# Kernel tuning notes

Measured on AMD Instinct MI355X. Metric: run time of the kernel, lower is better.

The kernel has to match this reference:

```python
import jax, jax.numpy as jnp
import numpy as np

B, CIN, COUT, T, K = 8, 64, 64, 16384, 127


def setup_inputs() -> dict:
    key = jax.random.key(0)
    kx, kw = jax.random.split(key)
    x = jax.random.normal(kx, (B, CIN, T), dtype=jnp.float32)
    sigma = np.sqrt(2.0 / (CIN * K + COUT)).astype(np.float32)
    W = jax.random.normal(kw, (COUT, CIN, K), dtype=jnp.float32) * sigma
    return {"x": x, "W": W}


def reference(x, W):
    # Full linear convolution via FFT (true convolution, matches
    # torchaudio.functional.fftconvolve), summed over in_channels,
    # then trimmed to mode='same' (output length == T, centered).
    T_ = x.shape[-1]
    K_ = W.shape[-1]
    n = T_ + K_ - 1  # linear-conv length, no circular wraparound
    Xf = jnp.fft.rfft(x, n=n)   # [B, Cin, nf] complex
    Wf = jnp.fft.rfft(W, n=n)   # [Cout, Cin, nf] complex
    # Batched complex multiply-accumulate over in_channels (single pass,
    # no per-output-channel redundant FFTs).
    Yf = jnp.einsum('bif,oif->bof', Xf, Wf)  # [B, Cout, nf]
    y_full = jnp.fft.irfft(Yf, n=n)          # [B, Cout, T+K-1]
    start = (K_ - 1) // 2                    # 'same': centered crop
    return y_full[..., start:start + T_]
```

## Files before the change

kernel.cpp:

```cpp
#include <hip/hip_runtime.h>

#define T_LEN 16384
#define CIN   64
#define COUT  64
#define KTAPS 127
#define TN    256
#define WROWS 383
#define WT_KS 4096

typedef __attribute__((ext_vector_type(8)))  __bf16 bf16x8;
typedef __attribute__((ext_vector_type(16))) float  f32x16;
typedef __attribute__((ext_vector_type(4)))  float  float4v;

__device__ inline unsigned short f2bf(float f) {
    unsigned u = __builtin_bit_cast(unsigned, f);
    u += 0x7fffu + ((u >> 16) & 1u);
    return (unsigned short)(u >> 16);
}

__global__ void wt_transform(const float* __restrict__ W,
                             unsigned short* __restrict__ Wt) {
    int tid = blockIdx.x * 256 + threadIdx.x;
    int o = tid >> 6, i = tid & 63;
    int j = i ^ ((o & 7) << 3);
    const float* src = W + tid * KTAPS;
    unsigned short* dst = Wt + o * 64 + j;
    for (int kp = 0; kp < KTAPS; ++kp)
        dst[kp * WT_KS] = f2bf(src[126 - kp]);
}

#define GLL16(g, l)                                                        \
    __builtin_amdgcn_global_load_lds(                                      \
        (const __attribute__((address_space(1))) void*)(g),                \
        (__attribute__((address_space(3))) void*)(l), 16, 0, 0)

__global__ __launch_bounds__(256, 2)
void conv_mfma(const float* __restrict__ x,
               const unsigned short* __restrict__ Wt,
               float* __restrict__ y) {
    __shared__ unsigned short xs[WROWS * 64];
    __shared__ unsigned short as_[2][WT_KS];

    const int tid = threadIdx.x;
    const int bb  = blockIdx.x >> 6;
    const int tt  = blockIdx.x & 63;
    const int t0  = tt * TN;

    {
        const int cin  = tid >> 2;
        const int wseg = (tid & 3) * 96;
        const float* xrow = x + (bb * CIN + cin) * T_LEN + (t0 - 64);
        for (int j = 0; j < 96; j += 4) {
            const int w = wseg + j;
            const int u = t0 - 64 + w;
            float4v v;
            if (u >= 0 && u + 3 < T_LEN) {
                v = *(const float4v*)(xrow + w);
            } else {
                v.x = (u + 0 >= 0 && u + 0 < T_LEN) ? xrow[w + 0] : 0.f;
                v.y = (u + 1 >= 0 && u + 1 < T_LEN) ? xrow[w + 1] : 0.f;
                v.z = (u + 2 >= 0 && u + 2 < T_LEN) ? xrow[w + 2] : 0.f;
                v.w = (u + 3 >= 0 && u + 3 < T_LEN) ? xrow[w + 3] : 0.f;
            }
            #pragma unroll
            for (int e = 0; e < 4; ++e) {
                const int we = w + e;
                if (we < WROWS) {
                    const float fv = (e == 0) ? v.x : (e == 1) ? v.y : (e == 2) ? v.z : v.w;
                    xs[we * 64 + (cin ^ ((we & 7) << 3))] = f2bf(fv);
                }
            }
        }
    }
    __syncthreads();

    const int lane   = tid & 63;
    const int wv     = tid >> 6;
    const int l31    = lane & 31;
    const int kg     = lane >> 5;
    const int twbase = wv * 64;
    const int h2     = kg ^ (l31 & 7);
    const int brow0  = twbase + l31 + 1;

    auto stageA = [&](int kp, unsigned short* buf) {
        const char* g = (const char*)(Wt + kp * WT_KS) + wv * 2048 + lane * 16;
        char* l = (char*)buf + wv * 2048 + lane * 16;
        GLL16(g, l);
        GLL16(g + 1024, l + 1024);
    };

    stageA(0, as_[0]);
    asm volatile("s_waitcnt vmcnt(0)" ::: "memory");
    __builtin_amdgcn_s_barrier();

    f32x16 acc[2][2] = {};

    for (int kp = 0; kp < KTAPS; ++kp) {
        const unsigned short* abuf = as_[kp & 1];
        if (kp + 1 < KTAPS) stageA(kp + 1, as_[(kp & 1) ^ 1]);

        const int w0    = brow0 + kp;
        const int h     = kg ^ (w0 & 7);
        const int base0 = w0 * 64;
        #pragma unroll
        for (int cc = 0; cc < 4; ++cc) {
            const int ach = (((cc << 1) ^ h2) << 3);
            bf16x8 a0 = *(const bf16x8*)(abuf + l31 * 64 + ach);
            bf16x8 a1 = *(const bf16x8*)(abuf + (l31 + 32) * 64 + ach);
            const int coff = (((cc << 1) ^ h) << 3);
            bf16x8 b0 = *(const bf16x8*)(xs + base0 + coff);
            bf16x8 b1 = *(const bf16x8*)(xs + base0 + 2048 + coff);
            acc[0][0] = __builtin_amdgcn_mfma_f32_32x32x16_bf16(a0, b0, acc[0][0], 0, 0, 0);
            acc[0][1] = __builtin_amdgcn_mfma_f32_32x32x16_bf16(a0, b1, acc[0][1], 0, 0, 0);
            acc[1][0] = __builtin_amdgcn_mfma_f32_32x32x16_bf16(a1, b0, acc[1][0], 0, 0, 0);
            acc[1][1] = __builtin_amdgcn_mfma_f32_32x32x16_bf16(a1, b1, acc[1][1], 0, 0, 0);
        }

        asm volatile("s_waitcnt vmcnt(0) lgkmcnt(0)" ::: "memory");
        __builtin_amdgcn_s_barrier();
    }

    const int ybase = (bb * COUT) * T_LEN;
    #pragma unroll
    for (int m = 0; m < 2; ++m) {
        #pragma unroll
        for (int n = 0; n < 2; ++n) {
            const int t = t0 + twbase + n * 32 + l31;
            #pragma unroll
            for (int r = 0; r < 16; ++r) {
                const int o = m * 32 + (r & 3) + 8 * (r >> 2) + 4 * kg;
                y[ybase + o * T_LEN + t] = acc[m][n][r];
            }
        }
    }
}

extern "C" void kernel_launch(void* const* d_in, const int* in_sizes, int n_in,
                              void* d_out, int out_size, void* d_ws, size_t ws_size,
                              hipStream_t stream) {
    const float* x = (const float*)d_in[0];
    const float* W = (const float*)d_in[1];
    float* yout = (float*)d_out;
    unsigned short* Wt = (unsigned short*)d_ws;

    wt_transform<<<16, 256, 0, stream>>>(W, Wt);

    const int grid = 8 * (T_LEN / TN);
    conv_mfma<<<grid, 256, 0, stream>>>(x, Wt, yout);
}
```

Baseline: 139.7 us.

## Double time tile per block and widen per-wave output tile to 64x128

Each block now covers 512 time steps instead of 256, and each wave computes a 2x4 grid of 32x32 MFMA tiles instead of 2x2. This reuses each A (weight) fragment across four B fragments and halves the number of weight tiles staged per output. The LDS swizzle changes to 4-element groups XORed with a 16-row pattern, fragments are assembled from two 8-byte loads, and the tap loop is unrolled by two with constant buffer indices. The trade-off is more accumulator registers, which forces occupancy down to one block per CU, and only 256 blocks in the grid.

```diff
diff --git a/kernel.cpp b/kernel.cpp
--- a/kernel.cpp
+++ b/kernel.cpp
@@ -4,8 +4,8 @@
 #define CIN   64
 #define COUT  64
 #define KTAPS 127
-#define TN    256
-#define WROWS 383
+#define TN    512
+#define XROWS 640
 #define WT_KS 4096
 
 typedef __attribute__((ext_vector_type(8)))  __bf16 bf16x8;
@@ -22,9 +22,9 @@
                              unsigned short* __restrict__ Wt) {
     int tid = blockIdx.x * 256 + threadIdx.x;
     int o = tid >> 6, i = tid & 63;
-    int j = i ^ ((o & 7) << 3);
+    int hw = o * 64 + (((i >> 2) ^ (o & 15)) << 2) + (i & 3);
     const float* src = W + tid * KTAPS;
-    unsigned short* dst = Wt + o * 64 + j;
+    unsigned short* dst = Wt + hw;
     for (int kp = 0; kp < KTAPS; ++kp)
         dst[kp * WT_KS] = f2bf(src[126 - kp]);
 }
@@ -34,97 +34,120 @@
         (const __attribute__((address_space(1))) void*)(g),                \
         (__attribute__((address_space(3))) void*)(l), 16, 0, 0)
 
-__global__ __launch_bounds__(256, 2)
+__global__ __launch_bounds__(256, 1)
 void conv_mfma(const float* __restrict__ x,
                const unsigned short* __restrict__ Wt,
                float* __restrict__ y) {
-    __shared__ unsigned short xs[WROWS * 64];
     __shared__ unsigned short as_[2][WT_KS];
+    __shared__ unsigned short xs[XROWS * 64];
 
     const int tid = threadIdx.x;
-    const int bb  = blockIdx.x >> 6;
-    const int tt  = blockIdx.x & 63;
+    const int bb  = blockIdx.x >> 5;
+    const int tt  = blockIdx.x & 31;
     const int t0  = tt * TN;
 
     {
-        const int cin  = tid >> 2;
-        const int wseg = (tid & 3) * 96;
-        const float* xrow = x + (bb * CIN + cin) * T_LEN + (t0 - 64);
-        for (int j = 0; j < 96; j += 4) {
-            const int w = wseg + j;
+        const int cin = tid >> 2;
+        const int s   = tid & 3;
+        const float* xrow = x + (bb * CIN + cin) * T_LEN;
+        const int p = cin >> 2, c3 = cin & 3;
+        for (int j = 0; j < 40; ++j) {
+            const int w = 16 * j + 4 * s;
             const int u = t0 - 64 + w;
             float4v v;
-            if (u >= 0 && u + 3 < T_LEN) {
-                v = *(const float4v*)(xrow + w);
+            if (u >= 0 && u + 4 <= T_LEN) {
+                v = *(const float4v*)(xrow + u);
             } else {
-                v.x = (u + 0 >= 0 && u + 0 < T_LEN) ? xrow[w + 0] : 0.f;
-                v.y = (u + 1 >= 0 && u + 1 < T_LEN) ? xrow[w + 1] : 0.f;
-                v.z = (u + 2 >= 0 && u + 2 < T_LEN) ? xrow[w + 2] : 0.f;
-                v.w = (u + 3 >= 0 && u + 3 < T_LEN) ? xrow[w + 3] : 0.f;
+                v.x = (u + 0 >= 0 && u + 0 < T_LEN) ? xrow[u + 0] : 0.f;
+                v.y = (u + 1 >= 0 && u + 1 < T_LEN) ? xrow[u + 1] : 0.f;
+                v.z = (u + 2 >= 0 && u + 2 < T_LEN) ? xrow[u + 2] : 0.f;
+                v.w = (u + 3 >= 0 && u + 3 < T_LEN) ? xrow[u + 3] : 0.f;
             }
             #pragma unroll
             for (int e = 0; e < 4; ++e) {
                 const int we = w + e;
-                if (we < WROWS) {
-                    const float fv = (e == 0) ? v.x : (e == 1) ? v.y : (e == 2) ? v.z : v.w;
-                    xs[we * 64 + (cin ^ ((we & 7) << 3))] = f2bf(fv);
-                }
+                const float fv = (e == 0) ? v.x : (e == 1) ? v.y : (e == 2) ? v.z : v.w;
+                xs[we * 64 + ((p ^ (we & 15)) << 2) + c3] = f2bf(fv);
             }
         }
     }
+
+    auto stageA = [&](int kp, int buf) {
+        const char* g = (const char*)(Wt + kp * WT_KS) + tid * 16;
+        char* l = (char*)(&as_[buf][0]) + tid * 16;
+        GLL16(g, l);
+        GLL16(g + 4096, l + 4096);
+    };
+
+    stageA(0, 0);
+    asm volatile("s_waitcnt vmcnt(0)" ::: "memory");
     __syncthreads();
 
     const int lane   = tid & 63;
     const int wv     = tid >> 6;
     const int l31    = lane & 31;
     const int kg     = lane >> 5;
-    const int twbase = wv * 64;
-    const int h2     = kg ^ (l31 & 7);
+    const int twbase = wv * 128;
     const int brow0  = twbase + l31 + 1;
 
-    auto stageA = [&](int kp, unsigned short* buf) {
-        const char* g = (const char*)(Wt + kp * WT_KS) + wv * 2048 + lane * 16;
-        char* l = (char*)buf + wv * 2048 + lane * 16;
-        GLL16(g, l);
-        GLL16(g + 1024, l + 1024);
+    int aoff[2][4][2];
+    #pragma unroll
+    for (int m = 0; m < 2; ++m)
+        #pragma unroll
+        for (int cc = 0; cc < 4; ++cc)
+            #pragma unroll
+            for (int h = 0; h < 2; ++h)
+                aoff[m][cc][h] = (l31 + 32 * m) * 128 +
+                                 (((4 * cc + 2 * kg + h) ^ (l31 & 15)) << 3);
+
+    const char* asbase = (const char*)&as_[0][0];
+    const char* xsbase = (const char*)&xs[0];
+
+    f32x16 acc[2][4] = {};
+
+    auto tap = [&](int kp, int buf) {
+        if (kp + 1 < KTAPS) stageA(kp + 1, buf ^ 1);
+        const int rb   = brow0 + kp;
+        const int rb15 = rb & 15;
+        const char* arow = asbase + buf * 8192;
+        const char* xrowp = xsbase + rb * 128;
+        #pragma unroll
+        for (int cc = 0; cc < 4; ++cc) {
+            bf16x8 a[2];
+            #pragma unroll
+            for (int m = 0; m < 2; ++m) {
+                uint2 lo = *(const uint2*)(arow + aoff[m][cc][0]);
+                uint2 hi = *(const uint2*)(arow + aoff[m][cc][1]);
+                uint4 t4 = {lo.x, lo.y, hi.x, hi.y};
+                a[m] = __builtin_bit_cast(bf16x8, t4);
+            }
+            const int o0 = (((4 * cc + 2 * kg + 0) ^ rb15) << 3);
+            const int o1 = (((4 * cc + 2 * kg + 1) ^ rb15) << 3);
+            #pragma unroll
+            for (int n = 0; n < 4; ++n) {
+                uint2 lo = *(const uint2*)(xrowp + n * 4096 + o0);
+                uint2 hi = *(const uint2*)(xrowp + n * 4096 + o1);
+                uint4 t4 = {lo.x, lo.y, hi.x, hi.y};
+                bf16x8 b = __builtin_bit_cast(bf16x8, t4);
+                acc[0][n] = __builtin_amdgcn_mfma_f32_32x32x16_bf16(a[0], b, acc[0][n], 0, 0, 0);
+                acc[1][n] = __builtin_amdgcn_mfma_f32_32x32x16_bf16(a[1], b, acc[1][n], 0, 0, 0);
+            }
+        }
+        asm volatile("s_waitcnt vmcnt(0)" ::: "memory");
+        __builtin_amdgcn_s_barrier();
     };
 
-    stageA(0, as_[0]);
-    asm volatile("s_waitcnt vmcnt(0)" ::: "memory");
-    __builtin_amdgcn_s_barrier();
-
-    f32x16 acc[2][2] = {};
-
-    for (int kp = 0; kp < KTAPS; ++kp) {
-        const unsigned short* abuf = as_[kp & 1];
-        if (kp + 1 < KTAPS) stageA(kp + 1, as_[(kp & 1) ^ 1]);
-
-        const int w0    = brow0 + kp;
-        const int h     = kg ^ (w0 & 7);
-        const int base0 = w0 * 64;
-        #pragma unroll
-        for (int cc = 0; cc < 4; ++cc) {
-            const int ach = (((cc << 1) ^ h2) << 3);
-            bf16x8 a0 = *(const bf16x8*)(abuf + l31 * 64 + ach);
-            bf16x8 a1 = *(const bf16x8*)(abuf + (l31 + 32) * 64 + ach);
-            const int coff = (((cc << 1) ^ h) << 3);
-            bf16x8 b0 = *(const bf16x8*)(xs + base0 + coff);
-            bf16x8 b1 = *(const bf16x8*)(xs + base0 + 2048 + coff);
-            acc[0][0] = __builtin_amdgcn_mfma_f32_32x32x16_bf16(a0, b0, acc[0][0], 0, 0, 0);
-            acc[0][1] = __builtin_amdgcn_mfma_f32_32x32x16_bf16(a0, b1, acc[0][1], 0, 0, 0);
-            acc[1][0] = __builtin_amdgcn_mfma_f32_32x32x16_bf16(a1, b0, acc[1][0], 0, 0, 0);
-            acc[1][1] = __builtin_amdgcn_mfma_f32_32x32x16_bf16(a1, b1, acc[1][1], 0, 0, 0);
-        }
-
-        asm volatile("s_waitcnt vmcnt(0) lgkmcnt(0)" ::: "memory");
-        __builtin_amdgcn_s_barrier();
+    for (int kp = 0; kp < KTAPS - 1; kp += 2) {
+        tap(kp + 0, 0);
+        tap(kp + 1, 1);
     }
+    tap(KTAPS - 1, 0);
 
     const int ybase = (bb * COUT) * T_LEN;
     #pragma unroll
     for (int m = 0; m < 2; ++m) {
         #pragma unroll
-        for (int n = 0; n < 2; ++n) {
+        for (int n = 0; n < 4; ++n) {
             const int t = t0 + twbase + n * 32 + l31;
             #pragma unroll
             for (int r = 0; r < 16; ++r) {
```

Result: slower. 149.3 us (+6.8%).
